# Performance work log

Measured on AMD Instinct MI355X. Metric: run time of the kernel, lower is better.

Reference implementation:

```python
import jax, jax.numpy as jnp
import numpy as np

EPS = 1e-5
DN = ('NCHW', 'OIHW', 'NCHW')


def conv3x3(x, w, b):
    y = jax.lax.conv_general_dilated(x, w, window_strides=(1, 1), padding='SAME',
                                     dimension_numbers=DN)
    return y + b[None, :, None, None]


def bn_relu(x, g, be, m, v):
    # inference-mode BatchNorm2d followed by ReLU, folded into one FMA
    inv = g / jnp.sqrt(v + EPS)
    return jax.nn.relu(x * inv[None, :, None, None] + (be - m * inv)[None, :, None, None])


def haar_idwt2(cA, cH, cV, cD):
    # pywt.idwt2(coeffs, 'db1'): cH = detail along rows (axis -2), cV = detail along cols (axis -1)
    # Exact Haar synthesis -> 2x2 pixel blocks (pixel-shuffle style, no CPU round-trip)
    p00 = (cA + cH + cV + cD) * 0.5  # (2i,   2j)
    p01 = (cA + cH - cV - cD) * 0.5  # (2i,   2j+1)
    p10 = (cA - cH + cV - cD) * 0.5  # (2i+1, 2j)
    p11 = (cA - cH - cV + cD) * 0.5  # (2i+1, 2j+1)
    B, C, H, W = cA.shape
    even = jnp.stack([p00, p01], axis=-1).reshape(B, C, H, 2 * W)
    odd = jnp.stack([p10, p11], axis=-1).reshape(B, C, H, 2 * W)
    return jnp.stack([even, odd], axis=-2).reshape(B, C, 2 * H, 2 * W)


def setup_inputs() -> dict:
    key = jax.random.key(0)
    ks = jax.random.split(key, 24)
    B, IN_C, OUT_C, H, W = 16, 128, 64, 64, 64
    d = {}
    d['x'] = jax.random.normal(ks[0], (B, IN_C, H, W), jnp.float32)
    d['s'] = jax.random.normal(ks[1], (B, OUT_C, 2 * H, 2 * W), jnp.float32)
    # input_convdwt: Conv(in_c -> 4*in_c) + BN
    d['w1'] = jax.random.normal(ks[2], (4 * IN_C, IN_C, 3, 3), jnp.float32) * 0.05
    d['b1'] = jax.random.normal(ks[3], (4 * IN_C,), jnp.float32) * 0.05
    d['g1'] = jax.random.uniform(ks[4], (4 * IN_C,), jnp.float32, 0.5, 1.5)
    d['be1'] = jax.random.normal(ks[5], (4 * IN_C,), jnp.float32) * 0.05
    d['m1'] = jax.random.normal(ks[6], (4 * IN_C,), jnp.float32) * 0.05
    d['v1'] = jax.random.uniform(ks[7], (4 * IN_C,), jnp.float32, 0.5, 1.5)
    # s_con: Conv(in_c -> out_c) + BN
    d['ws'] = jax.random.normal(ks[8], (OUT_C, IN_C, 3, 3), jnp.float32) * 0.05
    d['bs'] = jax.random.normal(ks[9], (OUT_C,), jnp.float32) * 0.05
    d['gs'] = jax.random.uniform(ks[10], (OUT_C,), jnp.float32, 0.5, 1.5)
    d['bes'] = jax.random.normal(ks[11], (OUT_C,), jnp.float32) * 0.05
    d['ms'] = jax.random.normal(ks[12], (OUT_C,), jnp.float32) * 0.05
    d['vs'] = jax.random.uniform(ks[13], (OUT_C,), jnp.float32, 0.5, 1.5)
    # conv: Conv(in_c -> out_c) + BN (applied to concat(s, s_out))
    d['w2'] = jax.random.normal(ks[14], (OUT_C, IN_C, 3, 3), jnp.float32) * 0.05
    d['b2'] = jax.random.normal(ks[15], (OUT_C,), jnp.float32) * 0.05
    d['g2'] = jax.random.uniform(ks[16], (OUT_C,), jnp.float32, 0.5, 1.5)
    d['be2'] = jax.random.normal(ks[17], (OUT_C,), jnp.float32) * 0.05
    d['m2'] = jax.random.normal(ks[18], (OUT_C,), jnp.float32) * 0.05
    d['v2'] = jax.random.uniform(ks[19], (OUT_C,), jnp.float32, 0.5, 1.5)
    return d


def reference(x, s, w1, b1, g1, be1, m1, v1,
              ws, bs, gs, bes, ms, vs,
              w2, b2, g2, be2, m2, v2):
    # input_convdwt: conv -> BN -> ReLU, channels in_c -> 4*in_c
    h = bn_relu(conv3x3(x, w1, b1), g1, be1, m1, v1)
    c = h.shape[1]
    q = c // 4
    cA, cH, cV, cD = h[:, :q], h[:, q:2 * q], h[:, 2 * q:3 * q], h[:, 3 * q:]
    idwt_out = haar_idwt2(cA, cH, cV, cD)  # (B, in_c, 2H, 2W)
    # skip-connection branch (s is not None)
    s_out = bn_relu(conv3x3(idwt_out, ws, bs), gs, bes, ms, vs)  # (B, out_c, 2H, 2W)
    concat = jnp.concatenate([s, s_out], axis=1)                  # (B, in_c, 2H, 2W)
    decoder_output = bn_relu(conv3x3(concat, w2, b2), g2, be2, m2, v2)
    return decoder_output
```

## Files before the change

### kernel.cpp

```cpp
#include <hip/hip_runtime.h>
#include <hip/hip_bf16.h>

typedef __attribute__((ext_vector_type(8))) short short8;
typedef __attribute__((ext_vector_type(4))) float f32x4;
typedef unsigned short u16;

#define EPSV 1e-5f

__device__ __forceinline__ u16 f2bf(float f) {
    __hip_bfloat16 h = __float2bfloat16(f);
    return *reinterpret_cast<u16*>(&h);
}

__global__ void cvt_kernel(const float* __restrict__ src, u16* __restrict__ dst,
                           int C, int H, int W, int units) {
    int u = blockIdx.x * 256 + threadIdx.x;
    if (u >= units) return;
    int kb = u & 3;
    int p  = u >> 2;
    int x  = p % W;  p /= W;
    int y  = p % H;  p /= H;
    int n  = p & 15;
    int cc = p >> 4;
    short8 v;
#pragma unroll
    for (int j = 0; j < 8; ++j)
        v[j] = (short)f2bf(src[(((size_t)n * C + cc * 32 + kb * 8 + j) * H + y) * W + x]);
    *(short8*)(dst + ((((size_t)cc * 16 + n) * H + y) * W + x) * 32 + kb * 8) = v;
}

__global__ void repack_w1_kernel(const float* __restrict__ w1, u16* __restrict__ wf) {
    int u = blockIdx.x * 256 + threadIdx.x;
    if (u >= 4 * 8 * 9 * 4 * 64) return;
    int l = u & 63;
    int r = u >> 6;
    int ciC = r & 3;  r >>= 2;
    int t   = r % 9;  r /= 9;
    int bt  = r & 7;
    int cc  = r >> 3;
    int co  = (bt >> 1) * 128 + cc * 32 + (bt & 1) * 16 + (l & 15);
    int ci0 = ciC * 32 + (l >> 4) * 8;
    short8 v;
#pragma unroll
    for (int e = 0; e < 8; ++e)
        v[e] = (short)f2bf(w1[((size_t)co * 128 + ci0 + e) * 9 + t]);
    *(short8*)(wf + (size_t)u * 8) = v;
}

__global__ void repack_wg_kernel(const float* __restrict__ w, u16* __restrict__ wf) {
    int u = blockIdx.x * 256 + threadIdx.x;
    if (u >= 4 * 9 * 4 * 64) return;
    int l = u & 63;
    int r = u >> 6;
    int ciC = r & 3;  r >>= 2;
    int t   = r % 9;
    int bt  = r / 9;
    int co  = bt * 16 + (l & 15);
    int ci0 = ciC * 32 + (l >> 4) * 8;
    short8 v;
#pragma unroll
    for (int e = 0; e < 8; ++e)
        v[e] = (short)f2bf(w[((size_t)co * 128 + ci0 + e) * 9 + t]);
    *(short8*)(wf + (size_t)u * 8) = v;
}

__global__ __launch_bounds__(256, 2)
void conv1_mfma_kernel(const u16* __restrict__ inb, const u16* __restrict__ wf,
                       const float* __restrict__ bb, const float* __restrict__ gg,
                       const float* __restrict__ bee, const float* __restrict__ mm,
                       const float* __restrict__ vv, u16* __restrict__ ob) {
    const int tile = blockIdx.x;
    const int cc   = blockIdx.y;
    const int n    = blockIdx.z;
    const int x0   = (tile & 3) * 16;
    const int y0   = (tile >> 2) * 8;
    const int tid  = threadIdx.x;
    const int lane = tid & 63;
    const int wid  = tid >> 6;
    const int wm   = wid >> 1;
    const int wc   = wid & 1;
    const int kb   = lane >> 4;
    const int xl   = lane & 15;

    __shared__ float4 lds4[720];
    const short8* ldsr = (const short8*)lds4;

    f32x4 acc[4][4];
#pragma unroll
    for (int j = 0; j < 4; ++j)
#pragma unroll
        for (int q = 0; q < 4; ++q) acc[j][q] = (f32x4){0.f, 0.f, 0.f, 0.f};

    float4 sreg[3];
    auto load_stage = [&](int ciC) {
#pragma unroll
        for (int p = 0; p < 3; ++p) {
            int e = p * 256 + tid;
            float4 v = make_float4(0.f, 0.f, 0.f, 0.f);
            if (e < 720) {
                int pix = e >> 2, ke = e & 3;
                int yy = pix / 18;
                int xx = pix - yy * 18;
                int gy = y0 - 1 + yy, gx = x0 - 1 + xx;
                if ((unsigned)gy < 64u && (unsigned)gx < 64u)
                    v = *(const float4*)(inb + ((((size_t)ciC * 16 + n) * 64 + gy) * 64 + gx) * 32 + ke * 8);
            }
            sreg[p] = v;
        }
    };
    auto write_stage = [&]() {
#pragma unroll
        for (int p = 0; p < 3; ++p) {
            int e = p * 256 + tid;
            if (e < 720) lds4[e ^ ((e >> 2) & 7)] = sreg[p];
        }
    };

    load_stage(0);
    for (int ciC = 0; ciC < 4; ++ciC) {
        write_stage();
        __syncthreads();
        if (ciC < 3) load_stage(ciC + 1);
#pragma unroll
        for (int dx = 0; dx < 3; ++dx) {
            short8 a[6];
#pragma unroll
            for (int r = 0; r < 6; ++r) {
                int pix = (wm * 4 + r) * 18 + xl + dx;
                int e = pix * 4 + kb;
                a[r] = ldsr[e ^ ((e >> 2) & 7)];
            }
#pragma unroll
            for (int dy = 0; dy < 3; ++dy) {
                const int t = dy * 3 + dx;
                short8 b[4];
#pragma unroll
                for (int q = 0; q < 4; ++q) {
                    int bt = q * 2 + wc;
                    b[q] = *(const short8*)(wf + ((size_t)(((cc * 8 + bt) * 9 + t) * 4 + ciC) * 64 + lane) * 8);
                }
#pragma unroll
                for (int j = 0; j < 4; ++j)
#pragma unroll
                    for (int q = 0; q < 4; ++q)
                        acc[j][q] = __builtin_amdgcn_mfma_f32_16x16x32_bf16(a[j + dy], b[q], acc[j][q], 0, 0, 0);
            }
        }
        __syncthreads();
    }

    float invq[4], shq[4];
#pragma unroll
    for (int q = 0; q < 4; ++q) {
        int co  = q * 128 + cc * 32 + wc * 16 + xl;
        float inv = gg[co] / sqrtf(vv[co] + EPSV);
        invq[q] = inv;
        shq[q]  = bb[co] * inv + bee[co] - mm[co] * inv;
    }
    const int c32 = wc * 16 + xl;
#pragma unroll
    for (int j = 0; j < 4; ++j) {
        int y = y0 + wm * 4 + j;
#pragma unroll
        for (int i = 0; i < 4; ++i) {
            float A_ = fmaxf(acc[j][0][i] * invq[0] + shq[0], 0.f);
            float H_ = fmaxf(acc[j][1][i] * invq[1] + shq[1], 0.f);
            float V_ = fmaxf(acc[j][2][i] * invq[2] + shq[2], 0.f);
            float D_ = fmaxf(acc[j][3][i] * invq[3] + shq[3], 0.f);
            float p00 = (A_ + H_ + V_ + D_) * 0.5f;
            float p01 = (A_ + H_ - V_ - D_) * 0.5f;
            float p10 = (A_ - H_ + V_ - D_) * 0.5f;
            float p11 = (A_ - H_ - V_ + D_) * 0.5f;
            int oy = 2 * y, ox = 2 * (x0 + kb * 4 + i);
            size_t base = ((((size_t)cc * 16 + n) * 128 + oy) * 128 + ox) * 32 + c32;
            ob[base]            = f2bf(p00);
            ob[base + 32]       = f2bf(p01);
            ob[base + 128 * 32] = f2bf(p10);
            ob[base + 128 * 32 + 32] = f2bf(p11);
        }
    }
}

template <bool FP32OUT>
__global__ __launch_bounds__(256, 2)
void convg_mfma_kernel(const u16* __restrict__ inb, const u16* __restrict__ wf,
                       const float* __restrict__ bb, const float* __restrict__ gg,
                       const float* __restrict__ bee, const float* __restrict__ mm,
                       const float* __restrict__ vv, u16* __restrict__ ob,
                       float* __restrict__ of) {
    const int tile = blockIdx.x;
    const int n    = blockIdx.y;
    const int x0   = (tile & 7) * 16;
    const int y0   = (tile >> 3) * 8;
    const int tid  = threadIdx.x;
    const int lane = tid & 63;
    const int wid  = tid >> 6;
    const int wm   = wid >> 1;
    const int wc   = wid & 1;
    const int kb   = lane >> 4;
    const int xl   = lane & 15;

    __shared__ float4 lds4[720];
    const short8* ldsr = (const short8*)lds4;

    f32x4 acc[4][2];
#pragma unroll
    for (int j = 0; j < 4; ++j)
#pragma unroll
        for (int cb = 0; cb < 2; ++cb) acc[j][cb] = (f32x4){0.f, 0.f, 0.f, 0.f};

    float4 sreg[3];
    auto load_stage = [&](int ciC) {
#pragma unroll
        for (int p = 0; p < 3; ++p) {
            int e = p * 256 + tid;
            float4 v = make_float4(0.f, 0.f, 0.f, 0.f);
            if (e < 720) {
                int pix = e >> 2, ke = e & 3;
                int yy = pix / 18;
                int xx = pix - yy * 18;
                int gy = y0 - 1 + yy, gx = x0 - 1 + xx;
                if ((unsigned)gy < 128u && (unsigned)gx < 128u)
                    v = *(const float4*)(inb + ((((size_t)ciC * 16 + n) * 128 + gy) * 128 + gx) * 32 + ke * 8);
            }
            sreg[p] = v;
        }
    };
    auto write_stage = [&]() {
#pragma unroll
        for (int p = 0; p < 3; ++p) {
            int e = p * 256 + tid;
            if (e < 720) lds4[e ^ ((e >> 2) & 7)] = sreg[p];
        }
    };

    load_stage(0);
    for (int ciC = 0; ciC < 4; ++ciC) {
        write_stage();
        __syncthreads();
        if (ciC < 3) load_stage(ciC + 1);
#pragma unroll
        for (int dx = 0; dx < 3; ++dx) {
            short8 a[6];
#pragma unroll
            for (int r = 0; r < 6; ++r) {
                int pix = (wm * 4 + r) * 18 + xl + dx;
                int e = pix * 4 + kb;
                a[r] = ldsr[e ^ ((e >> 2) & 7)];
            }
#pragma unroll
            for (int dy = 0; dy < 3; ++dy) {
                const int t = dy * 3 + dx;
                short8 b[2];
#pragma unroll
                for (int cb = 0; cb < 2; ++cb) {
                    int bt = wc * 2 + cb;
                    b[cb] = *(const short8*)(wf + ((size_t)((bt * 9 + t) * 4 + ciC) * 64 + lane) * 8);
                }
#pragma unroll
                for (int j = 0; j < 4; ++j)
#pragma unroll
                    for (int cb = 0; cb < 2; ++cb)
                        acc[j][cb] = __builtin_amdgcn_mfma_f32_16x16x32_bf16(a[j + dy], b[cb], acc[j][cb], 0, 0, 0);
            }
        }
        __syncthreads();
    }

#pragma unroll
    for (int cb = 0; cb < 2; ++cb) {
        int co = (wc * 2 + cb) * 16 + xl;
        float inv = gg[co] / sqrtf(vv[co] + EPSV);
        float sh  = bb[co] * inv + bee[co] - mm[co] * inv;
#pragma unroll
        for (int j = 0; j < 4; ++j) {
            int y = y0 + wm * 4 + j;
            if (FP32OUT) {
                float4 v4;
                v4.x = fmaxf(acc[j][cb][0] * inv + sh, 0.f);
                v4.y = fmaxf(acc[j][cb][1] * inv + sh, 0.f);
                v4.z = fmaxf(acc[j][cb][2] * inv + sh, 0.f);
                v4.w = fmaxf(acc[j][cb][3] * inv + sh, 0.f);
                *(float4*)&of[(((size_t)n * 64 + co) * 128 + y) * 128 + x0 + kb * 4] = v4;
            } else {
#pragma unroll
                for (int i = 0; i < 4; ++i) {
                    float val = fmaxf(acc[j][cb][i] * inv + sh, 0.f);
                    int xg = x0 + kb * 4 + i;
                    ob[((((size_t)(co >> 5) * 16 + n) * 128 + y) * 128 + xg) * 32 + (co & 31)] = f2bf(val);
                }
            }
        }
    }
}

extern "C" void kernel_launch(void* const* d_in, const int* in_sizes, int n_in,
                              void* d_out, int out_size, void* d_ws, size_t ws_size,
                              hipStream_t stream) {
    const float* x   = (const float*)d_in[0];
    const float* s   = (const float*)d_in[1];
    const float* w1  = (const float*)d_in[2];
    const float* b1  = (const float*)d_in[3];
    const float* g1  = (const float*)d_in[4];
    const float* be1 = (const float*)d_in[5];
    const float* m1  = (const float*)d_in[6];
    const float* v1  = (const float*)d_in[7];
    const float* wsw = (const float*)d_in[8];
    const float* bs  = (const float*)d_in[9];
    const float* gs  = (const float*)d_in[10];
    const float* bes = (const float*)d_in[11];
    const float* ms  = (const float*)d_in[12];
    const float* vs  = (const float*)d_in[13];
    const float* w2  = (const float*)d_in[14];
    const float* b2  = (const float*)d_in[15];
    const float* g2  = (const float*)d_in[16];
    const float* be2 = (const float*)d_in[17];
    const float* m2  = (const float*)d_in[18];
    const float* v2  = (const float*)d_in[19];
    float* out = (float*)d_out;

    char* wsp = (char*)d_ws;
    u16* xb   = (u16*)(wsp);
    u16* idwt = (u16*)(wsp + 16777216);
    u16* cat  = (u16*)(wsp + 16777216 + 67108864);
    u16* wf1  = (u16*)(wsp + 16777216 + 67108864 + 67108864);
    u16* wfS  = (u16*)(wsp + 16777216 + 67108864 + 67108864 + 1179648);
    u16* wf2  = (u16*)(wsp + 16777216 + 67108864 + 67108864 + 1179648 + 147456);

    cvt_kernel<<<dim3(4096), dim3(256), 0, stream>>>(x, xb, 128, 64, 64, 1048576);
    cvt_kernel<<<dim3(8192), dim3(256), 0, stream>>>(s, cat, 64, 128, 128, 2097152);
    repack_w1_kernel<<<dim3(288), dim3(256), 0, stream>>>(w1, wf1);
    repack_wg_kernel<<<dim3(36), dim3(256), 0, stream>>>(wsw, wfS);
    repack_wg_kernel<<<dim3(36), dim3(256), 0, stream>>>(w2, wf2);

    conv1_mfma_kernel<<<dim3(32, 4, 16), dim3(256), 0, stream>>>(
        xb, wf1, b1, g1, be1, m1, v1, idwt);

    convg_mfma_kernel<false><<<dim3(128, 16), dim3(256), 0, stream>>>(
        idwt, wfS, bs, gs, bes, ms, vs, cat + (size_t)2 * 16 * 128 * 128 * 32, nullptr);

    convg_mfma_kernel<true><<<dim3(128, 16), dim3(256), 0, stream>>>(
        cat, wf2, b2, g2, be2, m2, v2, nullptr, out);
}
```

Measured before the change: 220.2 us.

## Stage conv1 weights into double-buffered LDS via async global_load_lds

Conv1 MFMA fragments for the weights were read straight from global memory inside the inner loop. They are now prefetched into a double-buffered LDS region with global_load_lds, one dx slice ahead, so the loads overlap the MFMA work of the current slice. Synchronisation changes from __syncthreads to explicit s_waitcnt vmcnt/lgkmcnt plus s_barrier and sched_barrier. This adds about 48KB of LDS per block, which can lower occupancy, and more barriers per iteration. The hand-counted vmcnt values are fragile.

```diff
diff --git a/kernel.cpp b/kernel.cpp
--- a/kernel.cpp
+++ b/kernel.cpp
@@ -11,6 +11,11 @@
     __hip_bfloat16 h = __float2bfloat16(f);
     return *reinterpret_cast<u16*>(&h);
 }
+
+#define GLOAD_LDS16(g, l)                                                      \
+    __builtin_amdgcn_global_load_lds(                                          \
+        (const __attribute__((address_space(1))) void*)(g),                    \
+        (__attribute__((address_space(3))) void*)(l), 16, 0, 0)
 
 __global__ void cvt_kernel(const float* __restrict__ src, u16* __restrict__ dst,
                            int C, int H, int W, int units) {
@@ -83,7 +88,9 @@
     const int xl   = lane & 15;
 
     __shared__ float4 lds4[720];
-    const short8* ldsr = (const short8*)lds4;
+    __shared__ float4 wlds[2][1536];
+    const short8* ldsr  = (const short8*)lds4;
+    const short8* wldsr = (const short8*)wlds;
 
     f32x4 acc[4][4];
 #pragma unroll
@@ -115,14 +122,41 @@
             if (e < 720) lds4[e ^ ((e >> 2) & 7)] = sreg[p];
         }
     };
+    auto stage_w = [&](int ciC, int dx, int buf) {
+#pragma unroll
+        for (int i = 0; i < 6; ++i) {
+            int seg = wid * 6 + i;
+            int bt  = seg / 3;
+            int dy  = seg - bt * 3;
+            int t   = dy * 3 + dx;
+            const u16* gp = wf + (size_t)((cc * 8 + bt) * 9 + t) * 2048 + ciC * 512 + lane * 8;
+            GLOAD_LDS16(gp, &wlds[buf][seg * 64]);
+        }
+    };
 
     load_stage(0);
+    stage_w(0, 0, 0);
     for (int ciC = 0; ciC < 4; ++ciC) {
         write_stage();
-        __syncthreads();
+        asm volatile("s_waitcnt lgkmcnt(0)" ::: "memory");
+        __builtin_amdgcn_s_barrier();
+        __builtin_amdgcn_sched_barrier(0);
         if (ciC < 3) load_stage(ciC + 1);
 #pragma unroll
         for (int dx = 0; dx < 3; ++dx) {
+            const int cur = (ciC + dx) & 1;
+            if (dx == 0) {
+                if (ciC < 3) asm volatile("s_waitcnt vmcnt(3)" ::: "memory");
+                else         asm volatile("s_waitcnt vmcnt(0)" ::: "memory");
+            } else {
+                asm volatile("s_waitcnt vmcnt(0)" ::: "memory");
+            }
+            __builtin_amdgcn_sched_barrier(0);
+            __builtin_amdgcn_s_barrier();
+            __builtin_amdgcn_sched_barrier(0);
+            if (dx < 2)        stage_w(ciC, dx + 1, cur ^ 1);
+            else if (ciC < 3)  stage_w(ciC + 1, 0, cur ^ 1);
+
             short8 a[6];
 #pragma unroll
             for (int r = 0; r < 6; ++r) {
@@ -132,12 +166,11 @@
             }
 #pragma unroll
             for (int dy = 0; dy < 3; ++dy) {
-                const int t = dy * 3 + dx;
                 short8 b[4];
 #pragma unroll
                 for (int q = 0; q < 4; ++q) {
                     int bt = q * 2 + wc;
-                    b[q] = *(const short8*)(wf + ((size_t)(((cc * 8 + bt) * 9 + t) * 4 + ciC) * 64 + lane) * 8);
+                    b[q] = wldsr[cur * 1536 + (bt * 3 + dy) * 64 + lane];
                 }
 #pragma unroll
                 for (int j = 0; j < 4; ++j)
@@ -146,7 +179,7 @@
                         acc[j][q] = __builtin_amdgcn_mfma_f32_16x16x32_bf16(a[j + dy], b[q], acc[j][q], 0, 0, 0);
             }
         }
-        __syncthreads();
+        __builtin_amdgcn_s_barrier();
     }
 
     float invq[4], shq[4];
```

Result: faster. 213.2 us (-3.2%).
